# Performance work log

Measured on AMD Instinct MI355X. Metric: run time of the kernel, lower is better.

Reference implementation:

```python
import jax, jax.numpy as jnp
import numpy as np

COMPLEXES = 2048
RESX = 16
RESY = 16
RATE = 16
FEAT = 64


def setup_inputs() -> dict:
    key = jax.random.key(0)
    k1, k2, k3 = jax.random.split(key, 3)
    P = RATE * RATE  # samples per complex
    map_ = jax.random.normal(k1, (COMPLEXES, RESY, RESX, FEAT), dtype=jnp.float32)
    u = jax.random.uniform(k2, (COMPLEXES, P), dtype=jnp.float32)
    v = jax.random.uniform(k3, (COMPLEXES, P), dtype=jnp.float32)
    return {"map": map_, "u": u, "v": v}


def reference(map, u, v):
    # map: [complexes, resy, resx, feat]; u, v: [complexes, P] in [0,1]
    C, H, W, F = map.shape
    x = u * (W - 1)
    y = v * (H - 1)
    x0 = jnp.clip(jnp.floor(x).astype(jnp.int32), 0, W - 2)
    y0 = jnp.clip(jnp.floor(y).astype(jnp.int32), 0, H - 2)
    fx = (x - x0.astype(x.dtype))[..., None]  # [C, P, 1]
    fy = (y - y0.astype(y.dtype))[..., None]
    cidx = jnp.arange(C)[:, None]  # [C, 1] broadcast over samples
    g00 = map[cidx, y0, x0]          # [C, P, F]
    g01 = map[cidx, y0, x0 + 1]
    g10 = map[cidx, y0 + 1, x0]
    g11 = map[cidx, y0 + 1, x0 + 1]
    top = g00 * (1.0 - fx) + g01 * fx
    bot = g10 * (1.0 - fx) + g11 * fx
    return top * (1.0 - fy) + bot * fy  # [C, P, F]
```

## Files before the change

### kernel.cpp

```cpp
#include <hip/hip_runtime.h>

constexpr int C_ = 2048;
constexpr int H_ = 16;
constexpr int W_ = 16;
constexpr int F_ = 64;
constexpr int P_ = 256;
constexpr int MAP4 = H_ * W_ * F_ / 4;
constexpr int BLK = 1024;
constexpr int ITERS = P_ / (BLK / 16);

typedef __attribute__((address_space(3))) uint32_t lds_u32;
typedef const __attribute__((address_space(1))) uint32_t glb_u32;

__global__ __launch_bounds__(BLK, 8) void ngf_fetch_kernel(
    const float* __restrict__ map_,
    const float* __restrict__ u_,
    const float* __restrict__ v_,
    float* __restrict__ out_) {
  __shared__ float4 smap[MAP4];
  __shared__ float4 s_w[P_];
  __shared__ int    s_ix[P_];

  const int c = blockIdx.x;
  const int tid = threadIdx.x;

  const float4* __restrict__ gmap =
      (const float4*)(map_ + (size_t)c * (H_ * W_ * F_));
#pragma unroll
  for (int i = 0; i < MAP4 / BLK; ++i) {
    __builtin_amdgcn_global_load_lds((glb_u32*)(gmap + i * BLK + tid),
                                     (lds_u32*)(smap + i * BLK + tid),
                                     16, 0, 0);
  }

  if (tid < P_) {
    const float x = u_[(size_t)c * P_ + tid] * (float)(W_ - 1);
    const float y = v_[(size_t)c * P_ + tid] * (float)(H_ - 1);
    int x0 = (int)floorf(x);
    int y0 = (int)floorf(y);
    x0 = x0 < 0 ? 0 : (x0 > W_ - 2 ? W_ - 2 : x0);
    y0 = y0 < 0 ? 0 : (y0 > H_ - 2 ? H_ - 2 : y0);
    const float fx = x - (float)x0;
    const float fy = y - (float)y0;
    const float wx0 = 1.0f - fx;
    const float wy0 = 1.0f - fy;
    s_w[tid] = make_float4(wx0 * wy0, fx * wy0, wx0 * fy, fx * fy);
    s_ix[tid] = (y0 * W_ + x0) * (F_ / 4);
  }
  __syncthreads();

  float4* __restrict__ gout = (float4*)(out_ + (size_t)c * (P_ * F_));
  const int f = tid & 15;
  const int sbase = tid >> 4;

  float4 w[ITERS];
  int ix[ITERS];
#pragma unroll
  for (int it = 0; it < ITERS; ++it) {
    const int s = it * (BLK / 16) + sbase;
    w[it] = s_w[s];
    ix[it] = s_ix[s] + f;
  }

#pragma unroll
  for (int it = 0; it < ITERS; ++it) {
    const int s = it * (BLK / 16) + sbase;
    const float4 g00 = smap[ix[it]];
    const float4 g01 = smap[ix[it] + (F_ / 4)];
    const float4 g10 = smap[ix[it] + W_ * (F_ / 4)];
    const float4 g11 = smap[ix[it] + (W_ + 1) * (F_ / 4)];

    float4 r;
    r.x = g00.x * w[it].x + g01.x * w[it].y + g10.x * w[it].z + g11.x * w[it].w;
    r.y = g00.y * w[it].x + g01.y * w[it].y + g10.y * w[it].z + g11.y * w[it].w;
    r.z = g00.z * w[it].x + g01.z * w[it].y + g10.z * w[it].z + g11.z * w[it].w;
    r.w = g00.w * w[it].x + g01.w * w[it].y + g10.w * w[it].z + g11.w * w[it].w;

    gout[s * (F_ / 4) + f] = r;
  }
}

extern "C" void kernel_launch(void* const* d_in, const int* in_sizes, int n_in,
                              void* d_out, int out_size, void* d_ws, size_t ws_size,
                              hipStream_t stream) {
  const float* map_ = (const float*)d_in[0];
  const float* u_   = (const float*)d_in[1];
  const float* v_   = (const float*)d_in[2];
  float* out_ = (float*)d_out;

  ngf_fetch_kernel<<<C_, BLK, 0, stream>>>(map_, u_, v_, out_);
}
```

Measured before the change: 237.6 us.

## Persistent blocks with double-buffered LDS prefetch of next complex's map

Replaces one block per complex with 256 persistent blocks that each loop over 8 complexes. The next complex's map is loaded asynchronously into a second LDS buffer, and its u/v values are read while the current one is being interpolated, so load latency overlaps compute and stores. Output writes become nontemporal stores. In exchange, LDS use per block doubles and only 256 blocks run, which may leave CUs underused on a 256-CU part and reduces how many waves can hide latency.

```diff
diff --git a/kernel.cpp b/kernel.cpp
--- a/kernel.cpp
+++ b/kernel.cpp
@@ -7,76 +7,121 @@
 constexpr int P_ = 256;
 constexpr int MAP4 = H_ * W_ * F_ / 4;
 constexpr int BLK = 1024;
-constexpr int ITERS = P_ / (BLK / 16);
+constexpr int NBLOCKS = 256;
+constexpr int NC = C_ / NBLOCKS;
+constexpr int ITERS = P_ * 16 / BLK;
 
 typedef __attribute__((address_space(3))) uint32_t lds_u32;
 typedef const __attribute__((address_space(1))) uint32_t glb_u32;
+using f32x4 = __attribute__((ext_vector_type(4))) float;
 
-__global__ __launch_bounds__(BLK, 8) void ngf_fetch_kernel(
+__global__ __launch_bounds__(BLK, 4) void ngf_fetch_kernel(
     const float* __restrict__ map_,
     const float* __restrict__ u_,
     const float* __restrict__ v_,
     float* __restrict__ out_) {
-  __shared__ float4 smap[MAP4];
-  __shared__ float4 s_w[P_];
-  __shared__ int    s_ix[P_];
+  __shared__ float4 smap[2][MAP4];
+  __shared__ float4 s_w[2][P_];
+  __shared__ int    s_ix[2][P_];
 
-  const int c = blockIdx.x;
+  const int b = blockIdx.x;
   const int tid = threadIdx.x;
+  const int f = tid & 15;
+  const int sbase = tid >> 4;
 
-  const float4* __restrict__ gmap =
-      (const float4*)(map_ + (size_t)c * (H_ * W_ * F_));
+  {
+    const float4* __restrict__ g =
+        (const float4*)(map_ + (size_t)b * (H_ * W_ * F_));
 #pragma unroll
-  for (int i = 0; i < MAP4 / BLK; ++i) {
-    __builtin_amdgcn_global_load_lds((glb_u32*)(gmap + i * BLK + tid),
-                                     (lds_u32*)(smap + i * BLK + tid),
-                                     16, 0, 0);
-  }
-
-  if (tid < P_) {
-    const float x = u_[(size_t)c * P_ + tid] * (float)(W_ - 1);
-    const float y = v_[(size_t)c * P_ + tid] * (float)(H_ - 1);
-    int x0 = (int)floorf(x);
-    int y0 = (int)floorf(y);
-    x0 = x0 < 0 ? 0 : (x0 > W_ - 2 ? W_ - 2 : x0);
-    y0 = y0 < 0 ? 0 : (y0 > H_ - 2 ? H_ - 2 : y0);
-    const float fx = x - (float)x0;
-    const float fy = y - (float)y0;
-    const float wx0 = 1.0f - fx;
-    const float wy0 = 1.0f - fy;
-    s_w[tid] = make_float4(wx0 * wy0, fx * wy0, wx0 * fy, fx * fy);
-    s_ix[tid] = (y0 * W_ + x0) * (F_ / 4);
+    for (int k = 0; k < MAP4 / BLK; ++k) {
+      __builtin_amdgcn_global_load_lds((glb_u32*)(g + k * BLK + tid),
+                                       (lds_u32*)(&smap[0][k * BLK + tid]),
+                                       16, 0, 0);
+    }
+    if (tid < P_) {
+      const float x = u_[(size_t)b * P_ + tid] * (float)(W_ - 1);
+      const float y = v_[(size_t)b * P_ + tid] * (float)(H_ - 1);
+      int x0 = (int)floorf(x);
+      int y0 = (int)floorf(y);
+      x0 = x0 < 0 ? 0 : (x0 > W_ - 2 ? W_ - 2 : x0);
+      y0 = y0 < 0 ? 0 : (y0 > H_ - 2 ? H_ - 2 : y0);
+      const float fx = x - (float)x0;
+      const float fy = y - (float)y0;
+      const float wx0 = 1.0f - fx;
+      const float wy0 = 1.0f - fy;
+      s_w[0][tid] = make_float4(wx0 * wy0, fx * wy0, wx0 * fy, fx * fy);
+      s_ix[0][tid] = (y0 * W_ + x0) * (F_ / 4);
+    }
   }
   __syncthreads();
 
-  float4* __restrict__ gout = (float4*)(out_ + (size_t)c * (P_ * F_));
-  const int f = tid & 15;
-  const int sbase = tid >> 4;
+#pragma unroll
+  for (int i = 0; i < NC; ++i) {
+    const int cur = i & 1;
+    const int nxt = cur ^ 1;
+    const int c = i * NBLOCKS + b;
 
-  float4 w[ITERS];
-  int ix[ITERS];
+    if (i + 1 < NC) {
+      const int cn = (i + 1) * NBLOCKS + b;
+      const float4* __restrict__ g =
+          (const float4*)(map_ + (size_t)cn * (H_ * W_ * F_));
 #pragma unroll
-  for (int it = 0; it < ITERS; ++it) {
-    const int s = it * (BLK / 16) + sbase;
-    w[it] = s_w[s];
-    ix[it] = s_ix[s] + f;
-  }
+      for (int k = 0; k < MAP4 / BLK; ++k) {
+        __builtin_amdgcn_global_load_lds((glb_u32*)(g + k * BLK + tid),
+                                         (lds_u32*)(&smap[nxt][k * BLK + tid]),
+                                         16, 0, 0);
+      }
+    }
 
+    float un = 0.0f, vn = 0.0f;
+    if (i + 1 < NC && tid < P_) {
+      const int cn = (i + 1) * NBLOCKS + b;
+      un = u_[(size_t)cn * P_ + tid];
+      vn = v_[(size_t)cn * P_ + tid];
+    }
+
+    float4 w[ITERS];
+    int ix[ITERS];
 #pragma unroll
-  for (int it = 0; it < ITERS; ++it) {
-    const int s = it * (BLK / 16) + sbase;
-    const float4 g00 = smap[ix[it]];
-    const float4 g01 = smap[ix[it] + (F_ / 4)];
-    const float4 g10 = smap[ix[it] + W_ * (F_ / 4)];
-    const float4 g11 = smap[ix[it] + (W_ + 1) * (F_ / 4)];
+    for (int it = 0; it < ITERS; ++it) {
+      const int s = it * (BLK / 16) + sbase;
+      w[it] = s_w[cur][s];
+      ix[it] = s_ix[cur][s] + f;
+    }
+    float4* __restrict__ gout = (float4*)(out_ + (size_t)c * (P_ * F_));
+#pragma unroll
+    for (int it = 0; it < ITERS; ++it) {
+      const int s = it * (BLK / 16) + sbase;
+      const float4 g00 = smap[cur][ix[it]];
+      const float4 g01 = smap[cur][ix[it] + (F_ / 4)];
+      const float4 g10 = smap[cur][ix[it] + W_ * (F_ / 4)];
+      const float4 g11 = smap[cur][ix[it] + (W_ + 1) * (F_ / 4)];
 
-    float4 r;
-    r.x = g00.x * w[it].x + g01.x * w[it].y + g10.x * w[it].z + g11.x * w[it].w;
-    r.y = g00.y * w[it].x + g01.y * w[it].y + g10.y * w[it].z + g11.y * w[it].w;
-    r.z = g00.z * w[it].x + g01.z * w[it].y + g10.z * w[it].z + g11.z * w[it].w;
-    r.w = g00.w * w[it].x + g01.w * w[it].y + g10.w * w[it].z + g11.w * w[it].w;
+      f32x4 r;
+      r.x = g00.x * w[it].x + g01.x * w[it].y + g10.x * w[it].z + g11.x * w[it].w;
+      r.y = g00.y * w[it].x + g01.y * w[it].y + g10.y * w[it].z + g11.y * w[it].w;
+      r.z = g00.z * w[it].x + g01.z * w[it].y + g10.z * w[it].z + g11.z * w[it].w;
+      r.w = g00.w * w[it].x + g01.w * w[it].y + g10.w * w[it].z + g11.w * w[it].w;
 
-    gout[s * (F_ / 4) + f] = r;
+      __builtin_nontemporal_store(r, (f32x4*)(gout + s * (F_ / 4) + f));
+    }
+
+    if (i + 1 < NC && tid < P_) {
+      const float x = un * (float)(W_ - 1);
+      const float y = vn * (float)(H_ - 1);
+      int x0 = (int)floorf(x);
+      int y0 = (int)floorf(y);
+      x0 = x0 < 0 ? 0 : (x0 > W_ - 2 ? W_ - 2 : x0);
+      y0 = y0 < 0 ? 0 : (y0 > H_ - 2 ? H_ - 2 : y0);
+      const float fx = x - (float)x0;
+      const float fy = y - (float)y0;
+      const float wx0 = 1.0f - fx;
+      const float wy0 = 1.0f - fy;
+      s_w[nxt][tid] = make_float4(wx0 * wy0, fx * wy0, wx0 * fy, fx * fy);
+      s_ix[nxt][tid] = (y0 * W_ + x0) * (F_ / 4);
+    }
+
+    __syncthreads();
   }
 }
 
@@ -88,5 +133,5 @@
   const float* v_   = (const float*)d_in[2];
   float* out_ = (float*)d_out;
 
-  ngf_fetch_kernel<<<C_, BLK, 0, stream>>>(map_, u_, v_, out_);
+  ngf_fetch_kernel<<<NBLOCKS, BLK, 0, stream>>>(map_, u_, v_, out_);
 }
```

After: 239.5 us. Within noise of the previous version (+0.8%).

## Persistent blocks with double-buffered LDS staging and nontemporal output stores

Applied to the files above, without the earlier changes.

The kernel now launches 256 persistent blocks, each processing 8 complexes in turn. The map tile and interpolation coefficients for the next complex are prefetched into a second LDS buffer while the current one is computed and stored. Odd blocks are offset by one complex so that their load and store phases are staggered. Output writes use nontemporal stores to keep the write-once results from polluting cache. The trade-off is fewer blocks in flight and twice the LDS per block, which lowers occupancy and may leave some CUs idle.

```diff
diff --git a/kernel.cpp b/kernel.cpp
--- a/kernel.cpp
+++ b/kernel.cpp
@@ -7,76 +7,111 @@
 constexpr int P_ = 256;
 constexpr int MAP4 = H_ * W_ * F_ / 4;
 constexpr int BLK = 1024;
-constexpr int ITERS = P_ / (BLK / 16);
+constexpr int NBLOCKS = 256;
+constexpr int NC = C_ / NBLOCKS;
+constexpr int ITERS = 4;
 
 typedef __attribute__((address_space(3))) uint32_t lds_u32;
 typedef const __attribute__((address_space(1))) uint32_t glb_u32;
+using f32x4 = __attribute__((ext_vector_type(4))) float;
 
-__global__ __launch_bounds__(BLK, 8) void ngf_fetch_kernel(
+__global__ __launch_bounds__(BLK, 4) void ngf_fetch_kernel(
     const float* __restrict__ map_,
     const float* __restrict__ u_,
     const float* __restrict__ v_,
     float* __restrict__ out_) {
-  __shared__ float4 smap[MAP4];
-  __shared__ float4 s_w[P_];
-  __shared__ int    s_ix[P_];
+  __shared__ float4 smap[2][MAP4];
+  __shared__ float4 s_w[2][P_];
+  __shared__ int    s_ix[2][P_];
 
-  const int c = blockIdx.x;
+  const int b = blockIdx.x;
   const int tid = threadIdx.x;
-
-  const float4* __restrict__ gmap =
-      (const float4*)(map_ + (size_t)c * (H_ * W_ * F_));
-#pragma unroll
-  for (int i = 0; i < MAP4 / BLK; ++i) {
-    __builtin_amdgcn_global_load_lds((glb_u32*)(gmap + i * BLK + tid),
-                                     (lds_u32*)(smap + i * BLK + tid),
-                                     16, 0, 0);
-  }
-
-  if (tid < P_) {
-    const float x = u_[(size_t)c * P_ + tid] * (float)(W_ - 1);
-    const float y = v_[(size_t)c * P_ + tid] * (float)(H_ - 1);
-    int x0 = (int)floorf(x);
-    int y0 = (int)floorf(y);
-    x0 = x0 < 0 ? 0 : (x0 > W_ - 2 ? W_ - 2 : x0);
-    y0 = y0 < 0 ? 0 : (y0 > H_ - 2 ? H_ - 2 : y0);
-    const float fx = x - (float)x0;
-    const float fy = y - (float)y0;
-    const float wx0 = 1.0f - fx;
-    const float wy0 = 1.0f - fy;
-    s_w[tid] = make_float4(wx0 * wy0, fx * wy0, wx0 * fy, fx * fy);
-    s_ix[tid] = (y0 * W_ + x0) * (F_ / 4);
-  }
-  __syncthreads();
-
-  float4* __restrict__ gout = (float4*)(out_ + (size_t)c * (P_ * F_));
   const int f = tid & 15;
   const int sbase = tid >> 4;
 
-  float4 w[ITERS];
-  int ix[ITERS];
+  auto cidx = [&](int i) { return i * NBLOCKS + b; };
+
+  auto stage = [&](int c, int buf) {
+    const float4* __restrict__ g =
+        (const float4*)(map_ + (size_t)c * (H_ * W_ * F_));
 #pragma unroll
-  for (int it = 0; it < ITERS; ++it) {
-    const int s = it * (BLK / 16) + sbase;
-    w[it] = s_w[s];
-    ix[it] = s_ix[s] + f;
+    for (int k = 0; k < MAP4 / BLK; ++k) {
+      __builtin_amdgcn_global_load_lds((glb_u32*)(g + k * BLK + tid),
+                                       (lds_u32*)(&smap[buf][k * BLK + tid]),
+                                       16, 0, 0);
+    }
+  };
+
+  auto coeffs = [&](int c, int buf) {
+    if (tid < P_) {
+      const float x = u_[(size_t)c * P_ + tid] * (float)(W_ - 1);
+      const float y = v_[(size_t)c * P_ + tid] * (float)(H_ - 1);
+      int x0 = (int)floorf(x);
+      int y0 = (int)floorf(y);
+      x0 = x0 < 0 ? 0 : (x0 > W_ - 2 ? W_ - 2 : x0);
+      y0 = y0 < 0 ? 0 : (y0 > H_ - 2 ? H_ - 2 : y0);
+      const float fx = x - (float)x0;
+      const float fy = y - (float)y0;
+      const float wx0 = 1.0f - fx;
+      const float wy0 = 1.0f - fy;
+      s_w[buf][tid] = make_float4(wx0 * wy0, fx * wy0, wx0 * fy, fx * fy);
+      s_ix[buf][tid] = (y0 * W_ + x0) * (F_ / 4);
+    }
+  };
+
+  auto compute_store = [&](int c, int buf) {
+    float4 w[ITERS];
+    int ix[ITERS];
+#pragma unroll
+    for (int it = 0; it < ITERS; ++it) {
+      const int s = it * (BLK / 16) + sbase;
+      w[it] = s_w[buf][s];
+      ix[it] = s_ix[buf][s] + f;
+    }
+    float4* __restrict__ gout = (float4*)(out_ + (size_t)c * (P_ * F_));
+#pragma unroll
+    for (int it = 0; it < ITERS; ++it) {
+      const int s = it * (BLK / 16) + sbase;
+      const float4 g00 = smap[buf][ix[it]];
+      const float4 g01 = smap[buf][ix[it] + (F_ / 4)];
+      const float4 g10 = smap[buf][ix[it] + W_ * (F_ / 4)];
+      const float4 g11 = smap[buf][ix[it] + (W_ + 1) * (F_ / 4)];
+
+      f32x4 r;
+      r.x = g00.x * w[it].x + g01.x * w[it].y + g10.x * w[it].z + g11.x * w[it].w;
+      r.y = g00.y * w[it].x + g01.y * w[it].y + g10.y * w[it].z + g11.y * w[it].w;
+      r.z = g00.z * w[it].x + g01.z * w[it].y + g10.z * w[it].z + g11.z * w[it].w;
+      r.w = g00.w * w[it].x + g01.w * w[it].y + g10.w * w[it].z + g11.w * w[it].w;
+
+      __builtin_nontemporal_store(r, (f32x4*)(gout + s * (F_ / 4) + f));
+    }
+  };
+
+  int i = 0, cur = 0;
+  stage(cidx(0), 0);
+  coeffs(cidx(0), 0);
+  __syncthreads();
+
+  if (b & 1) {
+    compute_store(cidx(0), 0);
+    __syncthreads();
+    stage(cidx(1), 1);
+    coeffs(cidx(1), 1);
+    __syncthreads();
+    i = 1;
+    cur = 1;
   }
 
-#pragma unroll
-  for (int it = 0; it < ITERS; ++it) {
-    const int s = it * (BLK / 16) + sbase;
-    const float4 g00 = smap[ix[it]];
-    const float4 g01 = smap[ix[it] + (F_ / 4)];
-    const float4 g10 = smap[ix[it] + W_ * (F_ / 4)];
-    const float4 g11 = smap[ix[it] + (W_ + 1) * (F_ / 4)];
+  for (; i < NC; ++i) {
+    const int nxt = cur ^ 1;
+    if (i + 1 < NC) {
+      stage(cidx(i + 1), nxt);
+      coeffs(cidx(i + 1), nxt);
+    }
+    compute_store(cidx(i), cur);
 
-    float4 r;
-    r.x = g00.x * w[it].x + g01.x * w[it].y + g10.x * w[it].z + g11.x * w[it].w;
-    r.y = g00.y * w[it].x + g01.y * w[it].y + g10.y * w[it].z + g11.y * w[it].w;
-    r.z = g00.z * w[it].x + g01.z * w[it].y + g10.z * w[it].z + g11.z * w[it].w;
-    r.w = g00.w * w[it].x + g01.w * w[it].y + g10.w * w[it].z + g11.w * w[it].w;
-
-    gout[s * (F_ / 4) + f] = r;
+    __syncthreads();
+    cur = nxt;
   }
 }
 
@@ -88,5 +123,5 @@
   const float* v_   = (const float*)d_in[2];
   float* out_ = (float*)d_out;
 
-  ngf_fetch_kernel<<<C_, BLK, 0, stream>>>(map_, u_, v_, out_);
+  ngf_fetch_kernel<<<NBLOCKS, BLK, 0, stream>>>(map_, u_, v_, out_);
 }
```

After: 241.2 us. No clear change (+1.5%).
